# Kernel optimization log

Hardware: AMD Instinct MI355X
Metric: run time of the kernel (lower is better)

## Reference

```python
import jax, jax.numpy as jnp
import numpy as np

DIM = 1024
HEADS = 16
HEAD_DIM = DIM // HEADS
EPS = 1e-5


def layer_norm(x, w, b):
    # normalize over last dim (head_dim)
    mu = jnp.mean(x, axis=-1, keepdims=True)
    var = jnp.mean(jnp.square(x - mu), axis=-1, keepdims=True)
    return (x - mu) * jax.lax.rsqrt(var + EPS) * w + b


def setup_inputs() -> dict:
    key = jax.random.key(0)
    ks = jax.random.split(key, 8)
    B, N = 2, 2048
    x = jax.random.normal(ks[0], (B, N, DIM), dtype=jnp.float32)
    mask = jax.random.randint(ks[1], (B, 1, N, N), 0, 2) == 1  # True = masked out
    qkv_w = jax.random.normal(ks[2], (3 * DIM, DIM), dtype=jnp.float32) * (DIM ** -0.5)
    q_norm_w = jnp.ones((HEAD_DIM,), dtype=jnp.float32)
    q_norm_b = jnp.zeros((HEAD_DIM,), dtype=jnp.float32)
    k_norm_w = jnp.ones((HEAD_DIM,), dtype=jnp.float32)
    k_norm_b = jnp.zeros((HEAD_DIM,), dtype=jnp.float32)
    proj_w = jax.random.normal(ks[3], (DIM, DIM), dtype=jnp.float32) * (DIM ** -0.5)
    proj_b = jnp.zeros((DIM,), dtype=jnp.float32)
    return {"x": x, "mask": mask, "qkv_w": qkv_w,
            "q_norm_w": q_norm_w, "q_norm_b": q_norm_b,
            "k_norm_w": k_norm_w, "k_norm_b": k_norm_b,
            "proj_w": proj_w, "proj_b": proj_b}


def reference(x, mask, qkv_w, q_norm_w, q_norm_b, k_norm_w, k_norm_b, proj_w, proj_b):
    B, N, C = x.shape
    H, D = HEADS, HEAD_DIM
    scale = D ** -0.5
    # qkv projection (no bias), split into q,k,v of shape (B,H,N,D)
    qkv = (x @ qkv_w.T).reshape(B, N, 3, H, D).transpose(2, 0, 3, 1, 4)
    q, k, v = qkv[0], qkv[1], qkv[2]
    q = layer_norm(q, q_norm_w, q_norm_b)
    k = layer_norm(k, k_norm_w, k_norm_b)
    q = q * scale
    attn = jnp.einsum("bhnd,bhmd->bhnm", q, k)  # (B,H,N,N)
    attn = jnp.where(mask, -jnp.inf, attn)
    attn = jax.nn.softmax(attn, axis=-1)
    out = jnp.einsum("bhnm,bhmd->bhnd", attn, v)
    out = out.transpose(0, 2, 1, 3).reshape(B, N, C)
    return out @ proj_w.T + proj_b
```

## Files before the change

kernel.cpp:

```cpp
#include <hip/hip_runtime.h>
#include <hip/hip_bf16.h>
#include <math.h>

#define B_    2
#define N_    2048
#define DIM_  1024
#define H_    16
#define HD_   64
#define EPS_  1e-5f
#define SCALE_ 0.125f
#define LOG2E_ 1.4426950408889634f
#define MFIX_  14.0f

typedef __attribute__((ext_vector_type(8))) __bf16 bf16x8;
typedef __attribute__((ext_vector_type(8))) unsigned short ushort8;
typedef __attribute__((ext_vector_type(4))) float f32x4;
typedef __attribute__((ext_vector_type(4))) unsigned int uint4v;

__device__ __forceinline__ unsigned short f2bf(float x) {
    unsigned u = __builtin_bit_cast(unsigned, x);
    u += 0x7fff + ((u >> 16) & 1);
    return (unsigned short)(u >> 16);
}
__device__ __forceinline__ unsigned pk2bf(float a, float b) {
    unsigned ua = __builtin_bit_cast(unsigned, a) + 0x8000u;
    unsigned ub = __builtin_bit_cast(unsigned, b) + 0x8000u;
    return __builtin_amdgcn_perm(ub, ua, 0x07060302);
}
__device__ __forceinline__ unsigned cvtpk(float a, float b) {
    unsigned r;
    asm("v_cvt_pk_bf16_f32 %0, %1, %2" : "=v"(r) : "v"(a), "v"(b));
    return r;
}

__device__ __forceinline__ void gl_lds16(const void* g, void* l) {
    __builtin_amdgcn_global_load_lds(
        (const __attribute__((address_space(1))) void*)g,
        (__attribute__((address_space(3))) void*)l, 16, 0, 0);
}

__global__ __launch_bounds__(256) void cast_and_pack(
    const float* __restrict__ x, const float* __restrict__ qkvw,
    const float* __restrict__ pw, const int* __restrict__ mask,
    unsigned short* __restrict__ out, unsigned long long* __restrict__ bm) {
    const int bid = blockIdx.x;
    if (bid < 4096) {
        int i = (bid * 256 + threadIdx.x) * 8;
        const float* src;
        if (i < 4194304) src = x + i;
        else if (i < 7340032) src = qkvw + (i - 4194304);
        else src = pw + (i - 7340032);
        float4 v0 = *(const float4*)src;
        float4 v1 = *(const float4*)(src + 4);
        ushort8 r;
        r[0] = f2bf(v0.x); r[1] = f2bf(v0.y); r[2] = f2bf(v0.z); r[3] = f2bf(v0.w);
        r[4] = f2bf(v1.x); r[5] = f2bf(v1.y); r[6] = f2bf(v1.z); r[7] = f2bf(v1.w);
        *(ushort8*)(out + i) = r;
    } else {
        int w = (bid - 4096) * 4 + (threadIdx.x >> 6);
        int lane = threadIdx.x & 63;
        int mv = mask[(size_t)w * 64 + lane];
        unsigned long long bits = __ballot(mv != 0);
        if (lane == 0) bm[w] = bits;
    }
}

#define GWB                                                               \
    asm volatile("s_waitcnt vmcnt(0)" ::: "memory");                      \
    __builtin_amdgcn_s_barrier();                                         \
    __builtin_amdgcn_sched_barrier(0);

#define QSTAGE(BUF, K0)                                                   \
    {                                                                     \
        _Pragma("unroll")                                                 \
        for (int c = 0; c < 2; ++c) {                                     \
            int pbase = wave * 2048 + c * 1024;                           \
            int myofs = pbase + lane * 16;                                \
            int r = myofs >> 6;                                           \
            int kb = myofs & 63;                                          \
            gl_lds16((const char*)A + ((size_t)(row0 + r) * K + (K0)) * 2 + kb, \
                     (char*)As[BUF] + pbase);                             \
            gl_lds16((const char*)Bw + ((size_t)(col0 + r) * K + (K0)) * 2 + kb, \
                     (char*)Bs[BUF] + pbase);                             \
        }                                                                 \
    }

#define QCOMPUTE(BUF)                                                     \
    {                                                                     \
        bf16x8 af[4], bfr[4];                                             \
        _Pragma("unroll")                                                 \
        for (int i = 0; i < 4; ++i) {                                     \
            af[i] = *(const bf16x8*)&As[BUF][(wr * 64 + i * 16 + lcol) * 32 + \
                                            quad * 8];                    \
            bfr[i] = *(const bf16x8*)&Bs[BUF][(wc * 64 + i * 16 + lcol) * 32 + \
                                             quad * 8];                   \
        }                                                                 \
        __builtin_amdgcn_s_setprio(1);                                    \
        _Pragma("unroll")                                                 \
        for (int i = 0; i < 4; ++i)                                       \
            _Pragma("unroll")                                             \
            for (int j = 0; j < 4; ++j)                                   \
                acc[i][j] = __builtin_amdgcn_mfma_f32_16x16x32_bf16(      \
                    af[i], bfr[j], acc[i][j], 0, 0, 0);                   \
        __builtin_amdgcn_s_setprio(0);                                    \
    }

__global__ __launch_bounds__(256) void gemm_qkv_ln(
    const unsigned short* __restrict__ A, const unsigned short* __restrict__ Bw,
    const float* __restrict__ qnw, const float* __restrict__ qnb,
    const float* __restrict__ knw, const float* __restrict__ knb,
    unsigned short* __restrict__ qbuf, unsigned short* __restrict__ kbuf,
    unsigned short* __restrict__ vt) {
    const int K = DIM_;
    __shared__ unsigned short As[2][128 * 32];
    __shared__ unsigned short Bs[2][128 * 32];
    const int tid = threadIdx.x;
    const int wave = tid >> 6, lane = tid & 63;
    const int quad = lane >> 4, lcol = lane & 15;
    const int wr = wave >> 1, wc = wave & 1;
    const int row0 = blockIdx.y * 128, col0 = blockIdx.x * 128;

    f32x4 acc[4][4];
#pragma unroll
    for (int i = 0; i < 4; ++i)
#pragma unroll
        for (int j = 0; j < 4; ++j) acc[i][j] = (f32x4){0.f, 0.f, 0.f, 0.f};

    QSTAGE(0, 0)
    GWB
    for (int k0 = 0; k0 < K - 64; k0 += 64) {
        QSTAGE(1, k0 + 32)
        QCOMPUTE(0)
        GWB
        QSTAGE(0, k0 + 64)
        QCOMPUTE(1)
        GWB
    }
    QSTAGE(1, K - 32)
    QCOMPUTE(0)
    GWB
    QCOMPUTE(1)

    const int colbase = col0 + wc * 64;
    const int t = colbase >> 10;
    const int h = (colbase & 1023) >> 6;

    if (t < 2) {
        const float* wv = (t == 0) ? qnw : knw;
        const float* bv = (t == 0) ? qnb : knb;
        float wreg[4], breg[4];
#pragma unroll
        for (int j = 0; j < 4; ++j) {
            wreg[j] = wv[j * 16 + lcol];
            breg[j] = bv[j * 16 + lcol];
        }
        const float sc = (t == 0) ? (SCALE_ * LOG2E_) : 1.f;
        unsigned short* obase = (t == 0) ? qbuf : kbuf;
#pragma unroll
        for (int i = 0; i < 4; ++i) {
#pragma unroll
            for (int reg = 0; reg < 4; ++reg) {
                int row = row0 + wr * 64 + i * 16 + quad * 4 + reg;
                int bb = row >> 11, n = row & (N_ - 1);
                float v[4];
#pragma unroll
                for (int j = 0; j < 4; ++j) v[j] = acc[i][j][reg];
                float s = v[0] + v[1] + v[2] + v[3];
                s += __shfl_xor(s, 1);
                s += __shfl_xor(s, 2);
                s += __shfl_xor(s, 4);
                s += __shfl_xor(s, 8);
                float mu = s * (1.f / 64.f);
                float d[4], s2 = 0.f;
#pragma unroll
                for (int j = 0; j < 4; ++j) {
                    d[j] = v[j] - mu;
                    s2 += d[j] * d[j];
                }
                s2 += __shfl_xor(s2, 1);
                s2 += __shfl_xor(s2, 2);
                s2 += __shfl_xor(s2, 4);
                s2 += __shfl_xor(s2, 8);
                float r = rsqrtf(s2 * (1.f / 64.f) + EPS_);
                float o0 = (d[0] * r * wreg[0] + breg[0]) * sc;
                float o1 = (d[1] * r * wreg[1] + breg[1]) * sc;
                float o2 = (d[2] * r * wreg[2] + breg[2]) * sc;
                float o3 = (d[3] * r * wreg[3] + breg[3]) * sc;
                uint2 pk;
                pk.x = pk2bf(o0, o1);
                pk.y = pk2bf(o2, o3);
                *(uint2*)(obase + ((size_t)(bb * H_ + h) * N_ + n) * 64 +
                          lcol * 4) = pk;
            }
        }
    } else {
        const int rowb = row0 + wr * 64;
        const int bb = rowb >> 11;
        unsigned short* vtb =
            vt + ((size_t)(bb * H_ + h) * 64) * (size_t)N_ + (rowb & (N_ - 1));
#pragma unroll
        for (int i = 0; i < 4; ++i) {
            const int pos = (i >> 1) * 32 + quad * 8 + (i & 1) * 4;
#pragma unroll
            for (int jj = 0; jj < 4; ++jj) {
                uint2 pk;
                pk.x = pk2bf(acc[i][jj][0], acc[i][jj][1]);
                pk.y = pk2bf(acc[i][jj][2], acc[i][jj][3]);
                *(uint2*)(vtb + (size_t)(lcol + 16 * jj) * N_ + pos) = pk;
            }
        }
    }
}

#define PSTAGE(BUF, K0)                                                   \
    {                                                                     \
        _Pragma("unroll")                                                 \
        for (int pi = 0; pi < 3; ++pi) {                                  \
            int p = wave * 3 + pi;    \
            if (p < 8) {                                                  \
                int pbase = p * 1024;                                     \
                int myofs = pbase + lane * 16;                            \
                int r = myofs >> 6, kb = myofs & 63;                      \
                gl_lds16((const char*)A +                                 \
                             ((size_t)(row0 + r) * K + (K0)) * 2 + kb,    \
                         (char*)As[BUF] + pbase);                         \
            } else {                                                      \
                int pbase = (p - 8) * 1024;                               \
                int myofs = pbase + lane * 16;                            \
                int r = myofs >> 6, kb = myofs & 63;                      \
                gl_lds16((const char*)Bw +                                \
                             ((size_t)(col0 + r) * K + (K0)) * 2 + kb,    \
                         (char*)Bs[BUF] + pbase);                         \
            }                                                             \
        }                                                                 \
    }

#define PCOMPUTE(BUF)                                                     \
    {                                                                     \
        bf16x8 af[2], bfr[4];                                             \
        _Pragma("unroll")                                                 \
        for (int i = 0; i < 2; ++i)                                       \
            af[i] = *(const bf16x8*)&As[BUF][(wave * 32 + i * 16 + lcol) * 32 + \
                                            quad * 8];                    \
        _Pragma("unroll")                                                 \
        for (int j = 0; j < 4; ++j)                                       \
            bfr[j] = *(const bf16x8*)&Bs[BUF][(j * 16 + lcol) * 32 + quad * 8]; \
        __builtin_amdgcn_s_setprio(1);                                    \
        _Pragma("unroll")                                                 \
        for (int i = 0; i < 2; ++i)                                       \
            _Pragma("unroll")                                             \
            for (int j = 0; j < 4; ++j)                                   \
                acc[i][j] = __builtin_amdgcn_mfma_f32_16x16x32_bf16(      \
                    af[i], bfr[j], acc[i][j], 0, 0, 0);                   \
        __builtin_amdgcn_s_setprio(0);                                    \
    }

__global__ __launch_bounds__(256) void gemm_proj(
    const unsigned short* __restrict__ A, const unsigned short* __restrict__ Bw,
    const float* __restrict__ bias, float* __restrict__ Cout) {
    const int K = DIM_;
    __shared__ unsigned short As[2][128 * 32];
    __shared__ unsigned short Bs[2][64 * 32];
    const int tid = threadIdx.x;
    const int wave = tid >> 6, lane = tid & 63;
    const int quad = lane >> 4, lcol = lane & 15;
    const int row0 = blockIdx.y * 128, col0 = blockIdx.x * 64;

    f32x4 acc[2][4];
#pragma unroll
    for (int i = 0; i < 2; ++i)
#pragma unroll
        for (int j = 0; j < 4; ++j) acc[i][j] = (f32x4){0.f, 0.f, 0.f, 0.f};

    PSTAGE(0, 0)
    GWB
    for (int k0 = 0; k0 < K - 64; k0 += 64) {
        PSTAGE(1, k0 + 32)
        PCOMPUTE(0)
        GWB
        PSTAGE(0, k0 + 64)
        PCOMPUTE(1)
        GWB
    }
    PSTAGE(1, K - 32)
    PCOMPUTE(0)
    GWB
    PCOMPUTE(1)

#pragma unroll
    for (int i = 0; i < 2; ++i) {
#pragma unroll
        for (int j = 0; j < 4; ++j) {
            int col = col0 + j * 16 + lcol;
            float bv = bias[col];
#pragma unroll
            for (int reg = 0; reg < 4; ++reg) {
                int row = row0 + wave * 32 + i * 16 + quad * 4 + reg;
                Cout[(size_t)row * DIM_ + col] = acc[i][j][reg] + bv;
            }
        }
    }
}

#define WAITBAR(Ncnt)                                                     \
    asm volatile("s_waitcnt vmcnt(" #Ncnt ")" ::: "memory");              \
    __builtin_amdgcn_s_barrier();                                         \
    __builtin_amdgcn_sched_barrier(0);

#define ISSUE2(B0, B1)                                                    \
    {                                                                     \
        gl_lds16(kp0, (char*)Ks[B0] + kld0);                              \
        gl_lds16(kp1, (char*)Ks[B0] + kld1);                              \
        gl_lds16(vp0, (char*)Vts[B0] + kld0);                             \
        gl_lds16(vp1, (char*)Vts[B0] + kld1);                             \
        gl_lds16(kp0 + 8192, (char*)Ks[B1] + kld0);                       \
        gl_lds16(kp1 + 8192, (char*)Ks[B1] + kld1);                       \
        gl_lds16(vp0 + 128, (char*)Vts[B1] + kld0);                       \
        gl_lds16(vp1 + 128, (char*)Vts[B1] + kld1);                       \
        mm0[B0] = bmq0[0]; mm1[B0] = bmq1[0];                             \
        mm0[B1] = bmq0[1]; mm1[B1] = bmq1[1];                             \
        kp0 += 16384; kp1 += 16384; vp0 += 256; vp1 += 256;               \
        bmq0 += 2; bmq1 += 2;                                             \
    }

#define QKT(J, SACC, MWA, MWB)                                            \
    {                                                                     \
        unsigned long long mqa = (MWA) >> (quad * 4);                     \
        unsigned long long mqb = (MWB) >> (quad * 4);                     \
        unsigned ml[2][2];                                                \
        ml[0][0] = (unsigned)mqa; ml[0][1] = (unsigned)(mqa >> 32);       \
        ml[1][0] = (unsigned)mqb; ml[1][1] = (unsigned)(mqb >> 32);       \
        _Pragma("unroll")                                                 \
        for (int qf = 0; qf < 2; ++qf)                                    \
            _Pragma("unroll")                                             \
            for (int kt = 0; kt < 4; ++kt) {                              \
                unsigned word = ml[qf][kt >> 1];                          \
                _Pragma("unroll")                                         \
                for (int reg = 0; reg < 4; ++reg) {                       \
                    unsigned msk = (unsigned)(((int)(word <<              \
                        (31 - ((kt & 1) * 16 + reg)))) >> 31);            \
                    SACC[qf][kt][reg] = __builtin_bit_cast(float,         \
                        (msk & 0xc61c4000u) | (~msk & 0xc1600000u));      \
                }                                                         \
            }                                                             \
        __builtin_amdgcn_s_setprio(1);                                    \
        _Pragma("unroll")                                                 \
        for (int kt = 0; kt < 4; ++kt)                                    \
            _Pragma("unroll")                                             \
            for (int d0 = 0; d0 < 2; ++d0) {                              \
                bf16x8 ak = *(const bf16x8*)((const char*)Ks[J] +         \
                    (d0 * 4 + quad) * 1024 + kt * 256 + lofs);            \
                SACC[0][kt] = __builtin_amdgcn_mfma_f32_16x16x32_bf16(    \
                    ak, bq[0][d0], SACC[0][kt], 0, 0, 0);                 \
                SACC[1][kt] = __builtin_amdgcn_mfma_f32_16x16x32_bf16(    \
                    ak, bq[1][d0], SACC[1][kt], 0, 0, 0);                 \
            }                                                             \
        __builtin_amdgcn_s_setprio(0);                                    \
    }

#define SM(SACC, PK)                                                      \
    _Pragma("unroll")                                                     \
    for (int qf = 0; qf < 2; ++qf)                                        \
        _Pragma("unroll")                                                 \
        for (int kt = 0; kt < 4; ++kt) {                                  \
            float p0 = exp2f(SACC[qf][kt][0]);                            \
            float p1 = exp2f(SACC[qf][kt][1]);                            \
            float p2 = exp2f(SACC[qf][kt][2]);                            \
            float p3 = exp2f(SACC[qf][kt][3]);                            \
            PK[qf][kt].x = cvtpk(p0, p1);                                 \
            PK[qf][kt].y = cvtpk(p2, p3);                                 \
        }

#define PV(J, PK)                                                         \
    {                                                                     \
        __builtin_amdgcn_s_setprio(1);                                    \
        _Pragma("unroll")                                                 \
        for (int P = 0; P < 2; ++P) {                                     \
            bf16x8 bp[2];                                                 \
            _Pragma("unroll")                                             \
            for (int qf = 0; qf < 2; ++qf) {                              \
                uint4v bu;                                                \
                bu[0] = PK[qf][2 * P].x;  bu[1] = PK[qf][2 * P].y;        \
                bu[2] = PK[qf][2 * P + 1].x; bu[3] = PK[qf][2 * P + 1].y; \
                bp[qf] = __builtin_bit_cast(bf16x8, bu);                  \
                lacc[qf] = __builtin_amdgcn_mfma_f32_16x16x32_bf16(       \
                    ones, bp[qf], lacc[qf], 0, 0, 0);                     \
            }                                                             \
            _Pragma("unroll")                                             \
            for (int dt = 0; dt < 4; ++dt) {                              \
                bf16x8 va = *(const bf16x8*)((const char*)Vts[J] +        \
                    (P * 4 + quad) * 1024 + dt * 256 + lofs);             \
                oacc[0][dt] = __builtin_amdgcn_mfma_f32_16x16x32_bf16(    \
                    va, bp[0], oacc[0][dt], 0, 0, 0);                     \
                oacc[1][dt] = __builtin_amdgcn_mfma_f32_16x16x32_bf16(    \
                    va, bp[1], oacc[1][dt], 0, 0, 0);                     \
            }                                                             \
        }                                                                 \
        __builtin_amdgcn_s_setprio(0);                                    \
    }

#define PAIR(J0, J1)                                                      \
    {                                                                     \
        f32x4 saccA[2][4], saccB[2][4];                                   \
        uint2 pkA[2][4], pkB[2][4];                                       \
        QKT(J0, saccA, mm0[J0], mm1[J0])                                  \
        SM(saccA, pkA)                                                    \
        QKT(J1, saccB, mm0[J1], mm1[J1])                                  \
        PV(J0, pkA)                                                       \
        SM(saccB, pkB)                                                    \
        PV(J1, pkB)                                                       \
    }

__global__ __launch_bounds__(256, 2) void flash_attn_mfma9(
    const unsigned short* __restrict__ q, const unsigned short* __restrict__ k,
    const unsigned short* __restrict__ vt,
    const unsigned long long* __restrict__ bm, unsigned short* __restrict__ ao) {
    __shared__ unsigned short Qs[128 * 64];
    __shared__ unsigned short Ks[4][64 * 64];
    __shared__ unsigned short Vts[4][64 * 64];

    const int tid = threadIdx.x;
    const int wave = tid >> 6, lane = tid & 63;
    const int quad = lane >> 4, lcol = lane & 15;
    const int bh = blockIdx.y, b = bh >> 4, h = bh & 15;
    const int q0 = blockIdx.x * 128;
    const int lofs = (lcol ^ (quad * 2)) << 4;

    const char* kgbase = (const char*)k + (size_t)bh * N_ * 128;
    const char* vtbase = (const char*)vt + (size_t)bh * 64 * N_ * 2;

    const int c0 = wave * 2, c1 = c0 + 1;
    const int swz0 = (c0 & 3) * 2, swz1 = (c1 & 3) * 2;
    const int kld0 = c0 * 1024, kld1 = c1 * 1024;
    const char* kp0 = kgbase + (lane ^ swz0) * 128 + c0 * 16;
    const char* kp1 = kgbase + (lane ^ swz1) * 128 + c1 * 16;
    const char* vp0 = vtbase + (size_t)(lane ^ swz0) * (N_ * 2) + c0 * 16;
    const char* vp1 = vtbase + (size_t)(lane ^ swz1) * (N_ * 2) + c1 * 16;

    const unsigned long long* bmq0 =
        bm + ((size_t)b * N_ + q0 + wave * 32 + lcol) * 32;
    const unsigned long long* bmq1 = bmq0 + 16 * 32;
    unsigned long long mm0[4], mm1[4];

    {
        const char* qg = (const char*)(q + (size_t)(bh * N_ + q0) * 64);
#pragma unroll
        for (int c = 0; c < 4; ++c) {
            int base = wave * 4096 + c * 1024;
            gl_lds16(qg + base + lane * 16, (char*)Qs + base);
        }
    }
    asm volatile("" ::: "memory");
    __builtin_amdgcn_sched_barrier(0);
#pragma unroll
    for (int t = 0; t < 4; ++t) {
        gl_lds16(kp0, (char*)Ks[t] + kld0);
        gl_lds16(kp1, (char*)Ks[t] + kld1);
        gl_lds16(vp0, (char*)Vts[t] + kld0);
        gl_lds16(vp1, (char*)Vts[t] + kld1);
        mm0[t] = bmq0[t];
        mm1[t] = bmq1[t];
        kp0 += 8192; kp1 += 8192; vp0 += 128; vp1 += 128;
        __builtin_amdgcn_sched_barrier(0);
    }
    bmq0 += 4; bmq1 += 4;
    asm volatile("s_waitcnt vmcnt(24)" ::: "memory");
    __builtin_amdgcn_sched_barrier(0);

    bf16x8 bq[2][2];
#pragma unroll
    for (int qf = 0; qf < 2; ++qf)
#pragma unroll
        for (int d0 = 0; d0 < 2; ++d0)
            bq[qf][d0] = *(const bf16x8*)&Qs[(wave * 32 + qf * 16 + lcol) * 64 +
                                             d0 * 32 + quad * 8];

    ushort8 ot;
#pragma unroll
    for (int i = 0; i < 8; ++i) ot[i] = 0x3F80;
    const bf16x8 ones = __builtin_bit_cast(bf16x8, ot);

    f32x4 oacc[2][4];
#pragma unroll
    for (int qf = 0; qf < 2; ++qf)
#pragma unroll
        for (int dt = 0; dt < 4; ++dt) oacc[qf][dt] = (f32x4){0.f, 0.f, 0.f, 0.f};
    f32x4 lacc[2];
    lacc[0] = (f32x4){0.f, 0.f, 0.f, 0.f};
    lacc[1] = (f32x4){0.f, 0.f, 0.f, 0.f};

    WAITBAR(12)
    PAIR(0, 1)
    for (int g = 0; g < 7; ++g) {
        WAITBAR(0)
        ISSUE2(0, 1)
        PAIR(2, 3)
        WAITBAR(0)
        ISSUE2(2, 3)
        PAIR(0, 1)
    }
    WAITBAR(0)
    PAIR(2, 3)

#pragma unroll
    for (int qf = 0; qf < 2; ++qf) {
        float inv = 1.f / lacc[qf][0];
        int row = q0 + wave * 32 + qf * 16 + lcol;
        unsigned short* dst =
            ao + ((size_t)(b * N_ + row)) * DIM_ + h * 64 + quad * 4;
#pragma unroll
        for (int dt = 0; dt < 4; ++dt) {
            uint2 pko;
            pko.x = pk2bf(oacc[qf][dt][0] * inv, oacc[qf][dt][1] * inv);
            pko.y = pk2bf(oacc[qf][dt][2] * inv, oacc[qf][dt][3] * inv);
            *(uint2*)(dst + dt * 16) = pko;
        }
    }
}

extern "C" void kernel_launch(void* const* d_in, const int* in_sizes, int n_in,
                              void* d_out, int out_size, void* d_ws,
                              size_t ws_size, hipStream_t stream) {
    const float* x     = (const float*)d_in[0];
    const int*   mask  = (const int*)d_in[1];
    const float* qkv_w = (const float*)d_in[2];
    const float* qnw   = (const float*)d_in[3];
    const float* qnb   = (const float*)d_in[4];
    const float* knw   = (const float*)d_in[5];
    const float* knb   = (const float*)d_in[6];
    const float* pw    = (const float*)d_in[7];
    const float* pb    = (const float*)d_in[8];
    float* out = (float*)d_out;

    char* ws = (char*)d_ws;
    unsigned short* x_bf  = (unsigned short*)(ws + 0);
    unsigned short* qw_bf = (unsigned short*)(ws + 8388608);
    unsigned short* pw_bf = (unsigned short*)(ws + 14680064);
    unsigned short* qbuf  = (unsigned short*)(ws + 16777216);
    unsigned short* kbuf  = (unsigned short*)(ws + 25165824);
    unsigned short* ao_bnc= (unsigned short*)(ws + 33554432);
    unsigned short* vt    = (unsigned short*)(ws + 41943040);
    unsigned long long* bmask = (unsigned long long*)(ws + 50331648);

    cast_and_pack<<<4096 + 32768, 256, 0, stream>>>(
        x, qkv_w, pw, mask, x_bf, bmask);

    gemm_qkv_ln<<<dim3(3072 / 128, 4096 / 128), 256, 0, stream>>>(
        x_bf, qw_bf, qnw, qnb, knw, knb, qbuf, kbuf, vt);

    flash_attn_mfma9<<<dim3(N_ / 128, B_ * H_), 256, 0, stream>>>(
        qbuf, kbuf, vt, bmask, ao_bnc);

    gemm_proj<<<dim3(DIM_ / 64, 4096 / 128), 256, 0, stream>>>(
        ao_bnc, pw_bf, pb, out);
}
```

Baseline: 247.8 us.

## Triple-buffer GEMM K-loop and remap blocks for XCD-aware locality

```diff
diff --git a/kernel.cpp b/kernel.cpp
--- a/kernel.cpp
+++ b/kernel.cpp
@@ -65,8 +65,8 @@
     }
 }
 
-#define GWB                                                               \
-    asm volatile("s_waitcnt vmcnt(0)" ::: "memory");                      \
+#define GWAIT(Ncnt)                                                       \
+    asm volatile("s_waitcnt vmcnt(" #Ncnt ")" ::: "memory");              \
     __builtin_amdgcn_s_barrier();                                         \
     __builtin_amdgcn_sched_barrier(0);
 
@@ -112,13 +112,14 @@
     unsigned short* __restrict__ qbuf, unsigned short* __restrict__ kbuf,
     unsigned short* __restrict__ vt) {
     const int K = DIM_;
-    __shared__ unsigned short As[2][128 * 32];
-    __shared__ unsigned short Bs[2][128 * 32];
+    __shared__ unsigned short As[3][128 * 32];
+    __shared__ unsigned short Bs[3][128 * 32];
     const int tid = threadIdx.x;
     const int wave = tid >> 6, lane = tid & 63;
     const int quad = lane >> 4, lcol = lane & 15;
     const int wr = wave >> 1, wc = wave & 1;
-    const int row0 = blockIdx.y * 128, col0 = blockIdx.x * 128;
+    const int w0 = (blockIdx.x & 7) * 96 + (blockIdx.x >> 3);
+    const int row0 = (w0 / 24) * 128, col0 = (w0 % 24) * 128;
 
     f32x4 acc[4][4];
 #pragma unroll
@@ -127,19 +128,14 @@
         for (int j = 0; j < 4; ++j) acc[i][j] = (f32x4){0.f, 0.f, 0.f, 0.f};
 
     QSTAGE(0, 0)
-    GWB
-    for (int k0 = 0; k0 < K - 64; k0 += 64) {
-        QSTAGE(1, k0 + 32)
-        QCOMPUTE(0)
-        GWB
-        QSTAGE(0, k0 + 64)
-        QCOMPUTE(1)
-        GWB
-    }
-    QSTAGE(1, K - 32)
-    QCOMPUTE(0)
-    GWB
-    QCOMPUTE(1)
+    QSTAGE(1, 32)
+    for (int g = 0; g < 10; ++g) {
+        GWAIT(4) QSTAGE(2, (3 * g + 2) * 32) QCOMPUTE(0)
+        GWAIT(4) QSTAGE(0, (3 * g + 3) * 32) QCOMPUTE(1)
+        GWAIT(4) QSTAGE(1, (3 * g + 4) * 32) QCOMPUTE(2)
+    }
+    GWAIT(4) QCOMPUTE(0)
+    GWAIT(0) QCOMPUTE(1)
 
     const int colbase = col0 + wc * 64;
     const int t = colbase >> 10;
@@ -259,12 +255,13 @@
     const unsigned short* __restrict__ A, const unsigned short* __restrict__ Bw,
     const float* __restrict__ bias, float* __restrict__ Cout) {
     const int K = DIM_;
-    __shared__ unsigned short As[2][128 * 32];
-    __shared__ unsigned short Bs[2][64 * 32];
+    __shared__ unsigned short As[3][128 * 32];
+    __shared__ unsigned short Bs[3][64 * 32];
     const int tid = threadIdx.x;
     const int wave = tid >> 6, lane = tid & 63;
     const int quad = lane >> 4, lcol = lane & 15;
-    const int row0 = blockIdx.y * 128, col0 = blockIdx.x * 64;
+    const int w0 = (blockIdx.x & 7) * 64 + (blockIdx.x >> 3);
+    const int row0 = (w0 >> 4) * 128, col0 = (w0 & 15) * 64;
 
     f32x4 acc[2][4];
 #pragma unroll
@@ -273,19 +270,14 @@
         for (int j = 0; j < 4; ++j) acc[i][j] = (f32x4){0.f, 0.f, 0.f, 0.f};
 
     PSTAGE(0, 0)
-    GWB
-    for (int k0 = 0; k0 < K - 64; k0 += 64) {
-        PSTAGE(1, k0 + 32)
-        PCOMPUTE(0)
-        GWB
-        PSTAGE(0, k0 + 64)
-        PCOMPUTE(1)
-        GWB
-    }
-    PSTAGE(1, K - 32)
-    PCOMPUTE(0)
-    GWB
-    PCOMPUTE(1)
+    PSTAGE(1, 32)
+    for (int g = 0; g < 10; ++g) {
+        GWAIT(3) PSTAGE(2, (3 * g + 2) * 32) PCOMPUTE(0)
+        GWAIT(3) PSTAGE(0, (3 * g + 3) * 32) PCOMPUTE(1)
+        GWAIT(3) PSTAGE(1, (3 * g + 4) * 32) PCOMPUTE(2)
+    }
+    GWAIT(3) PCOMPUTE(0)
+    GWAIT(0) PCOMPUTE(1)
 
 #pragma unroll
     for (int i = 0; i < 2; ++i) {
@@ -545,12 +537,12 @@
     cast_and_pack<<<4096 + 32768, 256, 0, stream>>>(
         x, qkv_w, pw, mask, x_bf, bmask);
 
-    gemm_qkv_ln<<<dim3(3072 / 128, 4096 / 128), 256, 0, stream>>>(
+    gemm_qkv_ln<<<768, 256, 0, stream>>>(
         x_bf, qw_bf, qnw, qnb, knw, knb, qbuf, kbuf, vt);
 
     flash_attn_mfma9<<<dim3(N_ / 128, B_ * H_), 256, 0, stream>>>(
         qbuf, kbuf, vt, bmask, ao_bnc);
 
-    gemm_proj<<<dim3(DIM_ / 64, 4096 / 128), 256, 0, stream>>>(
+    gemm_proj<<<512, 256, 0, stream>>>(
         ao_bnc, pw_bf, pb, out);
 }
```

Result: slower. 260.9 us (+5.3%).
